# Kernel optimization log

Hardware: AMD Instinct MI355X
Metric: run time of the kernel (lower is better)

## Reference

```python
import jax, jax.numpy as jnp
import numpy as np

N_BINS = 64
N_SPLINE_DIMS = 3 * N_BINS - 1
N_GENES = 5000
N_GENES_OI = 5000
N_CUTS = 500_000
WINDOW_A, WINDOW_B = -10000.0, 10000.0
AB = WINDOW_B - WINDOW_A
MIN_BIN_WIDTH = 1e-3
MIN_BIN_HEIGHT = 1e-3
MIN_DERIVATIVE = 1e-3
# default init so that softplus(init) + min_derivative == 1 at the tails
DEFAULT_INIT = float(np.log(np.exp(1.0 - MIN_DERIVATIVE) - 1.0))
LOG_HALF = float(np.log(0.5))
LOG_AB = float(np.log(AB))


def setup_inputs() -> dict:
    key = jax.random.key(0)
    k1, k2, k3, k4 = jax.random.split(key, 4)
    value = jax.random.uniform(k1, (N_CUTS,), minval=WINDOW_A, maxval=WINDOW_B, dtype=jnp.float32)
    delta_spline = jax.random.normal(k2, (N_CUTS, N_SPLINE_DIMS), dtype=jnp.float32) * 0.1
    genes_oi = jax.random.randint(k3, (N_GENES_OI,), 0, N_GENES, dtype=jnp.int64 if jax.config.jax_enable_x64 else jnp.int32)
    local_gene_ix = jax.random.randint(k4, (N_CUTS,), 0, N_GENES_OI, dtype=jnp.int64 if jax.config.jax_enable_x64 else jnp.int32)
    spline_weight = jnp.full((N_GENES, N_SPLINE_DIMS), DEFAULT_INIT, dtype=jnp.float32)
    return {"value": value, "delta_spline": delta_spline, "genes_oi": genes_oi,
            "local_gene_ix": local_gene_ix, "spline_weight": spline_weight}


def _rqs_inverse(x, uw, uh, ud_padded):
    """Rational-quadratic spline, inverse pass, domain [-1,1]x[-1,1].
    x: (N,1); uw, uh: (N,1,K); ud_padded: (N,1,K+1)."""
    K = uw.shape[-1]
    pad = [(0, 0)] * (uw.ndim - 1) + [(1, 0)]

    w = jax.nn.softmax(uw, axis=-1)
    w = MIN_BIN_WIDTH + (1.0 - MIN_BIN_WIDTH * K) * w
    cw = jnp.pad(jnp.cumsum(w, axis=-1), pad)
    cw = 2.0 * cw - 1.0  # map [0,1] -> [-1,1]
    cw = cw.at[..., 0].set(-1.0).at[..., -1].set(1.0)
    w = cw[..., 1:] - cw[..., :-1]

    d = MIN_DERIVATIVE + jax.nn.softplus(ud_padded)  # (N,1,K+1)

    h = jax.nn.softmax(uh, axis=-1)
    h = MIN_BIN_HEIGHT + (1.0 - MIN_BIN_HEIGHT * K) * h
    ch = jnp.pad(jnp.cumsum(h, axis=-1), pad)
    ch = 2.0 * ch - 1.0
    ch = ch.at[..., 0].set(-1.0).at[..., -1].set(1.0)
    h = ch[..., 1:] - ch[..., :-1]

    # searchsorted over cumulative heights (inverse pass)
    bins = ch.at[..., -1].add(1e-6)
    idx = jnp.clip(jnp.sum((x[..., None] >= bins).astype(jnp.int32), axis=-1) - 1, 0, K - 1)

    def gather(t):
        return jnp.take_along_axis(t, idx[..., None], axis=-1)[..., 0]

    in_cw = gather(cw)
    in_w = gather(w)
    in_ch = gather(ch)
    in_h = gather(h)
    delta = gather(h / w)
    d0 = gather(d)
    d1 = jnp.take_along_axis(d, (idx + 1)[..., None], axis=-1)[..., 0]

    dy = x - in_ch
    s = d0 + d1 - 2.0 * delta
    a = dy * s + in_h * (delta - d0)
    b = in_h * d0 - dy * s
    c = -delta * dy
    disc = b * b - 4.0 * a * c
    root = (2.0 * c) / (-b - jnp.sqrt(jnp.maximum(disc, 0.0)))  # theta in [0,1]
    y = root * in_w + in_cw

    tom = root * (1.0 - root)
    denom = delta + s * tom
    deriv_num = (delta * delta) * (d1 * root * root + 2.0 * delta * tom + d0 * (1.0 - root) * (1.0 - root))
    logabsdet = -(jnp.log(deriv_num) - 2.0 * jnp.log(denom))  # negated for inverse
    return y, logabsdet


def reference(value, delta_spline, genes_oi, local_gene_ix, spline_weight):
    K = N_BINS
    spline = spline_weight[genes_oi][local_gene_ix] + delta_spline  # (N, 3K-1)
    uw = spline[:, None, :K]           # (N,1,K)
    uh = spline[:, None, K:2 * K]      # (N,1,K)
    ud = spline[:, None, 2 * K:]       # (N,1,K-1)

    x = (((value - WINDOW_A) / AB) - 0.5) * 2.0  # normalize to [-1,1]
    x = x[:, None]  # (N,1)

    inside = (x >= -1.0) & (x <= 1.0)
    ud_padded = jnp.pad(ud, [(0, 0), (0, 0), (1, 1)], constant_values=DEFAULT_INIT)
    xc = jnp.clip(x, -1.0, 1.0)
    _, logdet = _rqs_inverse(xc, uw, uh, ud_padded)
    logdet = jnp.where(inside, logdet, 0.0)  # linear tails: logabsdet = 0
    return LOG_HALF + logdet - LOG_AB  # (N,1)
```

## Files before the change

### kernel.cpp

```cpp
#include <hip/hip_runtime.h>

#define NSPL 191
constexpr float MIN_W = 0.001f, MIN_H = 0.001f, MIN_D = 0.001f;
constexpr float W_A = -10000.0f, AB = 20000.0f;
constexpr float LOG_HALF = -0.69314718055994530942f;
constexpr float LOG_AB   = 9.90348755253612804622f;

typedef float f4 __attribute__((ext_vector_type(4), aligned(4)));

template<int CTRL>
__device__ __forceinline__ float dpp_add(float x) {
    int t = __builtin_amdgcn_update_dpp(0, __float_as_int(x), CTRL, 0xf, 0xf, true);
    return x + __int_as_float(t);
}
template<int PAT>
__device__ __forceinline__ float swz_f(float x) {
    return __int_as_float(__builtin_amdgcn_ds_swizzle(__float_as_int(x), PAT));
}
template<int PAT>
__device__ __forceinline__ int swz_i(int x) {
    return __builtin_amdgcn_ds_swizzle(x, PAT);
}

__global__ __launch_bounds__(256, 4) void rqs_g16_kernel(
    const float* __restrict__ value,
    const float* __restrict__ dsg,
    const int*   __restrict__ genes_oi,
    const int*   __restrict__ lgi,
    const float* __restrict__ swg,
    float* __restrict__ out, int n)
{
    const int lane = threadIdx.x & 63;
    const int sub  = lane & 15;
    const int grp  = lane >> 4;
    const int wv   = threadIdx.x >> 6;
    const long ii  = (long)blockIdx.x * 16 + wv * 4 + grp;
    const int  ic  = (int)(ii < (long)n ? ii : (long)(n - 1));

    const int g = genes_oi[lgi[ic]];
    const float v = value[ic];

    const float* __restrict__ dsr = dsg + (long)ic * NSPL;
    const float* __restrict__ swr = swg + (long)g  * NSPL;

    const int cb = 4 * sub;
    const f4 dw = *(const f4*)(dsr + cb);
    const f4 dh = *(const f4*)(dsr + 64 + cb);
    const f4 ww = *(const f4*)(swr + cb);
    const f4 wh = *(const f4*)(swr + 64 + cb);

    float x = fmaf(v - W_A, 2.0f / AB, -1.0f);
    const bool inside = (x >= -1.0f) && (x <= 1.0f);
    x = fminf(fmaxf(x, -1.0f), 1.0f);

    const float ew0 = __expf(dw.x + ww.x), ew1 = __expf(dw.y + ww.y);
    const float ew2 = __expf(dw.z + ww.z), ew3 = __expf(dw.w + ww.w);
    const float eh0 = __expf(dh.x + wh.x), eh1 = __expf(dh.y + wh.y);
    const float eh2 = __expf(dh.z + wh.z), eh3 = __expf(dh.w + wh.w);

    float Sw = (ew0 + ew1) + (ew2 + ew3);
    Sw += swz_f<0x041F>(Sw); Sw += swz_f<0x081F>(Sw);
    Sw += swz_f<0x101F>(Sw); Sw += swz_f<0x201F>(Sw);

    float c0 = eh0, c1 = c0 + eh1, c2 = c1 + eh2, c3 = c2 + eh3;
    float t = c3;
    t = dpp_add<0x111>(t);
    t = dpp_add<0x112>(t);
    t = dpp_add<0x114>(t);
    t = dpp_add<0x118>(t);
    const float base = t - c3;
    c0 += base; c1 += base; c2 += base; c3 += base;
    const float Sh = swz_f<0x1F0>(c3);

    const float wsc2 = __fdividef(2.0f * (1.0f - 64.0f * MIN_W), Sw);
    const float hsc2 = __fdividef(2.0f * (1.0f - 64.0f * MIN_H), Sh);

    const float off2 = 2.0f * MIN_H;
    const float p1 = (float)(cb + 1);
    const float e0v = fmaf(hsc2, c0, fmaf(off2, p1,          -1.0f));
    const float e1v = fmaf(hsc2, c1, fmaf(off2, p1 + 1.0f,   -1.0f));
    const float e2v = fmaf(hsc2, c2, fmaf(off2, p1 + 2.0f,   -1.0f));
    float       e3v = fmaf(hsc2, c3, fmaf(off2, p1 + 3.0f,   -1.0f));
    if (sub == 15) e3v = 2.0f;
    int cnt = (x >= e0v) + (x >= e1v) + (x >= e2v) + (x >= e3v);
    cnt += swz_i<0x041F>(cnt); cnt += swz_i<0x081F>(cnt);
    cnt += swz_i<0x101F>(cnt); cnt += swz_i<0x201F>(cnt);
    const int idx = cnt;

    const int j  = idx - 1;
    const int q  = (j >> 2) & 15;
    const int ad = (grp * 16 + q) << 2;
    const float g0 = __int_as_float(__builtin_amdgcn_ds_bpermute(ad, __float_as_int(c0)));
    const float g1 = __int_as_float(__builtin_amdgcn_ds_bpermute(ad, __float_as_int(c1)));
    const float g2 = __int_as_float(__builtin_amdgcn_ds_bpermute(ad, __float_as_int(c2)));
    const float g3 = __int_as_float(__builtin_amdgcn_ds_bpermute(ad, __float_as_int(c3)));
    const int r = j & 3;
    float sel = (r == 0) ? g0 : (r == 1) ? g1 : (r == 2) ? g2 : g3;
    const float capEh = (idx == 0) ? 0.0f : sel;

    const float ew_i = __expf(dsr[idx]      + swr[idx]);
    const float eh_i = __expf(dsr[64 + idx] + swr[64 + idx]);
    const int cd0 = 127 + (idx > 1 ? idx : 1);
    const int cd1 = 128 + (idx < 62 ? idx : 62);
    const float u0 = dsr[cd0] + swr[cd0];
    const float u1 = dsr[cd1] + swr[cd1];
    const float d0 = (idx == 0)  ? 1.0f : (MIN_D + __logf(1.0f + __expf(u0)));
    const float d1 = (idx == 63) ? 1.0f : (MIN_D + __logf(1.0f + __expf(u1)));

    const float in_w = fmaf(wsc2, ew_i, 2.0f * MIN_W);
    const float in_h = fmaf(hsc2, eh_i, 2.0f * MIN_H);
    const float ch_l = fmaf(hsc2, capEh, fmaf(off2, (float)idx, -1.0f));

    const float delta = __fdividef(in_h, in_w);
    const float dy = x - ch_l;
    const float ss = d0 + d1 - 2.0f * delta;
    const float aa = dy * ss + in_h * (delta - d0);
    const float bb = in_h * d0 - dy * ss;
    const float cc = -delta * dy;
    const float disc = bb * bb - 4.0f * aa * cc;
    const float root = __fdividef(2.0f * cc, -bb - sqrtf(fmaxf(disc, 0.0f)));
    const float tom = root * (1.0f - root);
    const float denom = delta + ss * tom;
    const float omr = 1.0f - root;
    const float dnum = delta * delta * (d1 * root * root + 2.0f * delta * tom + d0 * omr * omr);
    const float logabsdet = -(__logf(dnum) - 2.0f * __logf(denom));

    if (sub == 0 && ii < (long)n)
        out[ii] = LOG_HALF + (inside ? logabsdet : 0.0f) - LOG_AB;
}

extern "C" void kernel_launch(void* const* d_in, const int* in_sizes, int n_in,
                              void* d_out, int out_size, void* d_ws, size_t ws_size,
                              hipStream_t stream) {
    const float* value         = (const float*)d_in[0];
    const float* delta_spline  = (const float*)d_in[1];
    const int*   genes_oi      = (const int*)d_in[2];
    const int*   local_gene_ix = (const int*)d_in[3];
    const float* spline_weight = (const float*)d_in[4];
    float* out = (float*)d_out;

    const int n = in_sizes[0];
    const int cuts_per_block = 16;
    const int blocks = (n + cuts_per_block - 1) / cuts_per_block;
    rqs_g16_kernel<<<blocks, 256, 0, stream>>>(
        value, delta_spline, genes_oi, local_gene_ix, spline_weight, out, n);
}
```

Measured before the change: 501.0 us.

## Stage per-cut spline terms in LDS instead of dependent global gathers

Each 16-lane group now loads the derivative parameters up front as vector loads. It writes the cumulative heights, width exponentials and summed derivative logits for its cut into shared memory. After the bin search, the selected values are read from LDS, replacing the ds_bpermute selection and six dependent scattered global loads with their extra exponentials. This targets the latency of the second round of global memory access, at the cost of 12 KB of LDS per block and deriving the bin height from a difference of cumulative sums.

```diff
diff --git a/kernel.cpp b/kernel.cpp
--- a/kernel.cpp
+++ b/kernel.cpp
@@ -6,7 +6,8 @@
 constexpr float LOG_HALF = -0.69314718055994530942f;
 constexpr float LOG_AB   = 9.90348755253612804622f;
 
-typedef float f4 __attribute__((ext_vector_type(4), aligned(4)));
+typedef float f4  __attribute__((ext_vector_type(4), aligned(4)));
+typedef float f4a __attribute__((ext_vector_type(4), aligned(16)));
 
 template<int CTRL>
 __device__ __forceinline__ float dpp_add(float x) {
@@ -30,24 +31,29 @@
     const float* __restrict__ swg,
     float* __restrict__ out, int n)
 {
-    const int lane = threadIdx.x & 63;
-    const int sub  = lane & 15;
-    const int grp  = lane >> 4;
-    const int wv   = threadIdx.x >> 6;
-    const long ii  = (long)blockIdx.x * 16 + wv * 4 + grp;
-    const int  ic  = (int)(ii < (long)n ? ii : (long)(n - 1));
+    __shared__ float lds[16 * 192];
+
+    const int sub = threadIdx.x & 15;
+    const int gid = threadIdx.x >> 4;
+    const long ii = (long)blockIdx.x * 16 + gid;
+    const int  ic = (int)(ii < (long)n ? ii : (long)(n - 1));
 
     const int g = genes_oi[lgi[ic]];
     const float v = value[ic];
 
     const float* __restrict__ dsr = dsg + (long)ic * NSPL;
     const float* __restrict__ swr = swg + (long)g  * NSPL;
+    float* __restrict__ gl = lds + gid * 192;
 
     const int cb = 4 * sub;
     const f4 dw = *(const f4*)(dsr + cb);
     const f4 dh = *(const f4*)(dsr + 64 + cb);
+    const f4 du = *(const f4*)(dsr + 127 + cb);
     const f4 ww = *(const f4*)(swr + cb);
     const f4 wh = *(const f4*)(swr + 64 + cb);
+    const f4 wu = *(const f4*)(swr + 127 + cb);
+
+    *(f4a*)(gl + 128 + cb) = (f4a){du.x + wu.x, du.y + wu.y, du.z + wu.z, du.w + wu.w};
 
     float x = fmaf(v - W_A, 2.0f / AB, -1.0f);
     const bool inside = (x >= -1.0f) && (x <= 1.0f);
@@ -57,6 +63,8 @@
     const float ew2 = __expf(dw.z + ww.z), ew3 = __expf(dw.w + ww.w);
     const float eh0 = __expf(dh.x + wh.x), eh1 = __expf(dh.y + wh.y);
     const float eh2 = __expf(dh.z + wh.z), eh3 = __expf(dh.w + wh.w);
+
+    *(f4a*)(gl + 64 + cb) = (f4a){ew0, ew1, ew2, ew3};
 
     float Sw = (ew0 + ew1) + (ew2 + ew3);
     Sw += swz_f<0x041F>(Sw); Sw += swz_f<0x081F>(Sw);
@@ -70,6 +78,9 @@
     t = dpp_add<0x118>(t);
     const float base = t - c3;
     c0 += base; c1 += base; c2 += base; c3 += base;
+
+    *(f4a*)(gl + cb) = (f4a){c0, c1, c2, c3};
+
     const float Sh = swz_f<0x1F0>(c3);
 
     const float wsc2 = __fdividef(2.0f * (1.0f - 64.0f * MIN_W), Sw);
@@ -77,35 +88,25 @@
 
     const float off2 = 2.0f * MIN_H;
     const float p1 = (float)(cb + 1);
-    const float e0v = fmaf(hsc2, c0, fmaf(off2, p1,          -1.0f));
-    const float e1v = fmaf(hsc2, c1, fmaf(off2, p1 + 1.0f,   -1.0f));
-    const float e2v = fmaf(hsc2, c2, fmaf(off2, p1 + 2.0f,   -1.0f));
-    float       e3v = fmaf(hsc2, c3, fmaf(off2, p1 + 3.0f,   -1.0f));
+    const float e0v = fmaf(hsc2, c0, fmaf(off2, p1,        -1.0f));
+    const float e1v = fmaf(hsc2, c1, fmaf(off2, p1 + 1.0f, -1.0f));
+    const float e2v = fmaf(hsc2, c2, fmaf(off2, p1 + 2.0f, -1.0f));
+    float       e3v = fmaf(hsc2, c3, fmaf(off2, p1 + 3.0f, -1.0f));
     if (sub == 15) e3v = 2.0f;
     int cnt = (x >= e0v) + (x >= e1v) + (x >= e2v) + (x >= e3v);
     cnt += swz_i<0x041F>(cnt); cnt += swz_i<0x081F>(cnt);
     cnt += swz_i<0x101F>(cnt); cnt += swz_i<0x201F>(cnt);
     const int idx = cnt;
 
-    const int j  = idx - 1;
-    const int q  = (j >> 2) & 15;
-    const int ad = (grp * 16 + q) << 2;
-    const float g0 = __int_as_float(__builtin_amdgcn_ds_bpermute(ad, __float_as_int(c0)));
-    const float g1 = __int_as_float(__builtin_amdgcn_ds_bpermute(ad, __float_as_int(c1)));
-    const float g2 = __int_as_float(__builtin_amdgcn_ds_bpermute(ad, __float_as_int(c2)));
-    const float g3 = __int_as_float(__builtin_amdgcn_ds_bpermute(ad, __float_as_int(c3)));
-    const int r = j & 3;
-    float sel = (r == 0) ? g0 : (r == 1) ? g1 : (r == 2) ? g2 : g3;
-    const float capEh = (idx == 0) ? 0.0f : sel;
-
-    const float ew_i = __expf(dsr[idx]      + swr[idx]);
-    const float eh_i = __expf(dsr[64 + idx] + swr[64 + idx]);
-    const int cd0 = 127 + (idx > 1 ? idx : 1);
-    const int cd1 = 128 + (idx < 62 ? idx : 62);
-    const float u0 = dsr[cd0] + swr[cd0];
-    const float u1 = dsr[cd1] + swr[cd1];
-    const float d0 = (idx == 0)  ? 1.0f : (MIN_D + __logf(1.0f + __expf(u0)));
-    const float d1 = (idx == 63) ? 1.0f : (MIN_D + __logf(1.0f + __expf(u1)));
+    const float capEh_r = gl[(idx > 0) ? (idx - 1) : 0];
+    const float capEh   = (idx == 0) ? 0.0f : capEh_r;
+    const float C_idx   = gl[idx];
+    const float eh_i    = C_idx - capEh;
+    const float ew_i    = gl[64 + idx];
+    const float u_d0    = gl[128 + idx];
+    const float u_d1    = gl[128 + ((idx + 1) & 63)];
+    const float d0 = (idx == 0)  ? 1.0f : (MIN_D + __logf(1.0f + __expf(u_d0)));
+    const float d1 = (idx == 63) ? 1.0f : (MIN_D + __logf(1.0f + __expf(u_d1)));
 
     const float in_w = fmaf(wsc2, ew_i, 2.0f * MIN_W);
     const float in_h = fmaf(hsc2, eh_i, 2.0f * MIN_H);
```

Result: no change. 499.9 us (-0.2%).
